# Kernel optimization log

Hardware: AMD Instinct MI355X
Metric: run time of the kernel (lower is better)

## Reference

```python
import jax, jax.numpy as jnp
import numpy as np

# ---- configuration (matches init_kwargs) ----
B, C_IO, T = 2, 64, 4096
PATCH = 2
W0, W1 = 512, 1024           # widths
D_DN, D_MID = 2, 4           # depths per level
DH = 64                      # dim per head
WIN = 128                    # local attention window
MAP = 1024                   # mapping_dim
DFF_MAP = 1024               # mapping_d_ff
FF_MULT = 2                  # GEGLU ff_mult in local levels
H_DN = W0 // DH              # 8 heads
H_MID = W1 // DH             # 16 heads


def _n(key, shape, s=0.02):
    return jax.random.normal(key, shape, jnp.float32) * s


def setup_inputs() -> dict:
    key = jax.random.key(0)
    ks = iter(jax.random.split(key, 64))
    p = {}
    p['x'] = jax.random.normal(next(ks), (B, C_IO, T), jnp.float32)
    p['t'] = jax.random.uniform(next(ks), (B,), jnp.float32)
    p['time_w'] = jax.random.normal(next(ks), (MAP // 2, 1), jnp.float32)
    p['time_in_w'] = _n(next(ks), (MAP, MAP))
    p['map_in_s'] = jnp.ones((MAP,), jnp.float32)
    p['map_norm_s'] = jnp.ones((2, MAP), jnp.float32)
    p['map_up_w'] = _n(next(ks), (2, MAP, 2 * DFF_MAP))
    p['map_down_w'] = _n(next(ks), (2, DFF_MAP, MAP))
    p['map_out_s'] = jnp.ones((MAP,), jnp.float32)
    p['patch_in_w'] = _n(next(ks), (C_IO * PATCH, W0))
    p['dn_anorm_w'] = _n(next(ks), (D_DN, MAP, W0))
    p['dn_qkv_w'] = _n(next(ks), (D_DN, W0, 3 * W0))
    p['dn_o_w'] = _n(next(ks), (D_DN, W0, W0))
    p['dn_fnorm_w'] = _n(next(ks), (D_DN, MAP, W0))
    p['dn_ff1_w'] = _n(next(ks), (D_DN, W0, 2 * FF_MULT * W0))
    p['dn_ff2_w'] = _n(next(ks), (D_DN, FF_MULT * W0, W0))
    p['merge_w'] = _n(next(ks), (W0 * 2, W1))
    p['mid_map_w'] = _n(next(ks), (MAP, W1))
    p['mid_pin_w'] = _n(next(ks), (W1, W1))
    p['mid_pout_w'] = _n(next(ks), (W1, W1))
    p['mid_ln1_g'] = jnp.ones((D_MID, W1), jnp.float32)
    p['mid_ln1_b'] = jnp.zeros((D_MID, W1), jnp.float32)
    p['mid_qkv_w'] = _n(next(ks), (D_MID, W1, 3 * W1))
    p['mid_o_w'] = _n(next(ks), (D_MID, W1, W1))
    p['mid_ln2_g'] = jnp.ones((D_MID, W1), jnp.float32)
    p['mid_ln2_b'] = jnp.zeros((D_MID, W1), jnp.float32)
    p['mid_ff1_w'] = _n(next(ks), (D_MID, W1, 8 * W1))
    p['mid_ff2_w'] = _n(next(ks), (D_MID, 4 * W1, W1))
    p['mid_fn_g'] = jnp.ones((W1,), jnp.float32)
    p['mid_fn_b'] = jnp.zeros((W1,), jnp.float32)
    p['split_w'] = _n(next(ks), (W1, W0 * 2))
    p['split_fac'] = jnp.full((1,), 0.5, jnp.float32)
    p['up_anorm_w'] = _n(next(ks), (D_DN, MAP, W0))
    p['up_qkv_w'] = _n(next(ks), (D_DN, W0, 3 * W0))
    p['up_o_w'] = _n(next(ks), (D_DN, W0, W0))
    p['up_fnorm_w'] = _n(next(ks), (D_DN, MAP, W0))
    p['up_ff1_w'] = _n(next(ks), (D_DN, W0, 2 * FF_MULT * W0))
    p['up_ff2_w'] = _n(next(ks), (D_DN, FF_MULT * W0, W0))
    p['out_norm_s'] = jnp.ones((W0,), jnp.float32)
    p['patch_out_w'] = _n(next(ks), (W0, C_IO * PATCH))
    return p


def rmsnorm(x, scale, eps=1e-6):
    ms = jnp.mean(jnp.square(x), -1, keepdims=True)
    return x * (scale * jax.lax.rsqrt(ms + eps))


def layernorm(x, g, b, eps=1e-5):
    m = jnp.mean(x, -1, keepdims=True)
    v = jnp.mean(jnp.square(x - m), -1, keepdims=True)
    return (x - m) * jax.lax.rsqrt(v + eps) * g + b


def rope_tables(S, D):
    inv = 1.0 / (10000.0 ** (jnp.arange(0, D, 2, dtype=jnp.float32) / D))
    ang = jnp.arange(S, dtype=jnp.float32)[:, None] * inv  # [S, D/2]
    return jnp.cos(ang), jnp.sin(ang)


def apply_rope(x, cos, sin):
    # x: [B,H,S,D], contiguous-half rotation
    x1, x2 = jnp.split(x, 2, -1)
    return jnp.concatenate([x1 * cos - x2 * sin, x2 * cos + x1 * sin], -1)


def heads_split(x, h):
    Bx, S, C = x.shape
    return x.reshape(Bx, S, h, C // h).transpose(0, 2, 1, 3)


def heads_merge(x):
    Bx, h, S, D = x.shape
    return x.transpose(0, 2, 1, 3).reshape(Bx, S, h * D)


def local_attn(q, k, v, w):
    # non-causal sliding-window attention: each query window attends to
    # [prev, self, next] windows (look_backward=1, look_forward=1)
    Bx, H, S, D = q.shape
    nw = S // w
    qw = q.reshape(Bx, H, nw, w, D)
    def ctx(tn):
        tw = tn.reshape(Bx, H, nw, w, D)
        pad = jnp.pad(tw, ((0, 0), (0, 0), (1, 1), (0, 0), (0, 0)))
        return jnp.concatenate([pad[:, :, :-2], pad[:, :, 1:-1], pad[:, :, 2:]], 3)  # [B,H,nw,3w,D]
    kw, vw = ctx(k), ctx(v)
    s = jnp.einsum('bhnqd,bhnkd->bhnqk', qw * (D ** -0.5), kw)
    valid = jnp.ones((nw, 3 * w), bool).at[0, :w].set(False).at[-1, 2 * w:].set(False)
    s = jnp.where(valid[None, None, :, None, :], s, jnp.finfo(s.dtype).min)
    a = jax.nn.softmax(s, -1)
    return jnp.einsum('bhnqk,bhnkd->bhnqd', a, vw).reshape(Bx, H, S, D)


def token_merge(x, w, r=2):
    # 'b (n r) c -> b n (c r)' then linear
    Bx, S, C = x.shape
    x = x.reshape(Bx, S // r, r, C).transpose(0, 1, 3, 2).reshape(Bx, S // r, C * r)
    return x @ w


def token_split(x, w, r=2):
    # linear then 'b n (c r) -> b (n r) c'
    y = x @ w
    Bx, n, CR = y.shape
    C = CR // r
    return y.reshape(Bx, n, C, r).transpose(0, 1, 3, 2).reshape(Bx, n * r, C)


def mapping(e, in_s, norm_s, up_w, down_w, out_s):
    x = rmsnorm(e, in_s)
    for l in range(up_w.shape[0]):
        h = rmsnorm(x, norm_s[l])
        a, g = jnp.split(h @ up_w[l], 2, -1)
        x = x + (a * jax.nn.gelu(g)) @ down_w[l]
    return rmsnorm(x, out_s)


def local_level(x, cond, anorm, qkv_w, o_w, fnorm, ff1, ff2, heads, win):
    Bx, S, C = x.shape
    D = C // heads
    cos, sin = rope_tables(S, D)
    for l in range(qkv_w.shape[0]):
        h = rmsnorm(x, 1.0 + (cond @ anorm[l])[:, None, :])  # AdaRMSNorm
        q, k, v = jnp.split(h @ qkv_w[l], 3, -1)
        q, k, v = heads_split(q, heads), heads_split(k, heads), heads_split(v, heads)
        q, k = apply_rope(q, cos, sin), apply_rope(k, cos, sin)
        x = x + heads_merge(local_attn(q, k, v, win)) @ o_w[l]
        h = rmsnorm(x, 1.0 + (cond @ fnorm[l])[:, None, :])
        a, g = jnp.split(h @ ff1[l], 2, -1)
        x = x + (a * jax.nn.gelu(g)) @ ff2[l]  # GEGLU FF
    return x


def mid_level(x, ln1g, ln1b, qkv_w, o_w, ln2g, ln2b, ff1, ff2, fng, fnb, heads):
    Bx, S, C = x.shape
    D = C // heads
    cos, sin = rope_tables(S, D)
    for l in range(qkv_w.shape[0]):
        h = layernorm(x, ln1g[l], ln1b[l])
        q, k, v = jnp.split(h @ qkv_w[l], 3, -1)
        q, k, v = heads_split(q, heads), heads_split(k, heads), heads_split(v, heads)
        q, k = apply_rope(q, cos, sin), apply_rope(k, cos, sin)
        s = jnp.einsum('bhqd,bhkd->bhqk', q * (D ** -0.5), k)
        o = jnp.einsum('bhqk,bhkd->bhqd', jax.nn.softmax(s, -1), v)
        x = x + heads_merge(o) @ o_w[l]
        h = layernorm(x, ln2g[l], ln2b[l])
        a, g = jnp.split(h @ ff1[l], 2, -1)
        x = x + (a * jax.nn.silu(g)) @ ff2[l]  # SwiGLU FF
    return layernorm(x, fng, fnb)


def _forward(x, t, time_w, time_in_w, map_in_s, map_norm_s, map_up_w, map_down_w, map_out_s,
             patch_in_w, dn_anorm_w, dn_qkv_w, dn_o_w, dn_fnorm_w, dn_ff1_w, dn_ff2_w,
             merge_w, mid_map_w, mid_pin_w, mid_pout_w, mid_ln1_g, mid_ln1_b, mid_qkv_w,
             mid_o_w, mid_ln2_g, mid_ln2_b, mid_ff1_w, mid_ff2_w, mid_fn_g, mid_fn_b,
             split_w, split_fac, up_anorm_w, up_qkv_w, up_o_w, up_fnorm_w, up_ff1_w,
             up_ff2_w, out_norm_s, patch_out_w):
    h = jnp.swapaxes(x, 1, 2)                      # [B,T,C_io]
    h = token_merge(h, patch_in_w, PATCH)          # [B, T/2, W0]
    f = 2.0 * jnp.pi * (t[:, None] @ time_w.T)     # Fourier features
    temb = jnp.concatenate([jnp.cos(f), jnp.sin(f)], -1) @ time_in_w
    cond = mapping(temb, map_in_s, map_norm_s, map_up_w, map_down_w, map_out_s)  # [B,MAP]
    h = local_level(h, cond, dn_anorm_w, dn_qkv_w, dn_o_w, dn_fnorm_w, dn_ff1_w, dn_ff2_w, H_DN, WIN)
    skip = h
    h = token_merge(h, merge_w)                    # [B, T/4, W1]
    h = h @ mid_pin_w
    pre = (cond @ mid_map_w)[:, None, :]           # prepended mapping token
    h = jnp.concatenate([pre, h], 1)
    h = mid_level(h, mid_ln1_g, mid_ln1_b, mid_qkv_w, mid_o_w, mid_ln2_g, mid_ln2_b,
                  mid_ff1_w, mid_ff2_w, mid_fn_g, mid_fn_b, H_MID)
    h = (h @ mid_pout_w)[:, 1:, :]
    h = token_split(h, split_w)                    # back to [B, T/2, W0]
    h = skip + split_fac * (h - skip)              # lerp skip fusion
    h = local_level(h, cond, up_anorm_w, up_qkv_w, up_o_w, up_fnorm_w, up_ff1_w, up_ff2_w, H_DN, WIN)
    h = rmsnorm(h, out_norm_s)
    h = token_split(h, patch_out_w, PATCH)         # [B,T,C_io]
    return jnp.swapaxes(h, 1, 2)


def reference(x, t, time_w, time_in_w, map_in_s, map_norm_s, map_up_w, map_down_w, map_out_s,
              patch_in_w, dn_anorm_w, dn_qkv_w, dn_o_w, dn_fnorm_w, dn_ff1_w, dn_ff2_w,
              merge_w, mid_map_w, mid_pin_w, mid_pout_w, mid_ln1_g, mid_ln1_b, mid_qkv_w,
              mid_o_w, mid_ln2_g, mid_ln2_b, mid_ff1_w, mid_ff2_w, mid_fn_g, mid_fn_b,
              split_w, split_fac, up_anorm_w, up_qkv_w, up_o_w, up_fnorm_w, up_ff1_w,
              up_ff2_w, out_norm_s, patch_out_w):
    return _forward(x, t, time_w, time_in_w, map_in_s, map_norm_s, map_up_w, map_down_w, map_out_s,
                    patch_in_w, dn_anorm_w, dn_qkv_w, dn_o_w, dn_fnorm_w, dn_ff1_w, dn_ff2_w,
                    merge_w, mid_map_w, mid_pin_w, mid_pout_w, mid_ln1_g, mid_ln1_b, mid_qkv_w,
                    mid_o_w, mid_ln2_g, mid_ln2_b, mid_ff1_w, mid_ff2_w, mid_fn_g, mid_fn_b,
                    split_w, split_fac, up_anorm_w, up_qkv_w, up_o_w, up_fnorm_w, up_ff1_w,
                    up_ff2_w, out_norm_s, patch_out_w)
```

## Files before the change

### kernel.cpp

```cpp
#include <hip/hip_runtime.h>
#include <math.h>

#define BB   2
#define CIO  64
#define TT   4096
#define S0   2048
#define W0   512
#define HDN  8
#define SM   1025
#define SMP  1088
#define W1   1024
#define HMID 16
#define WIN  128
#define NW   16
#define MAPD 1024
#define KSPL 16
#define PKCAP 8396800L

typedef _Float16 f16;
typedef _Float16 half8 __attribute__((ext_vector_type(8)));
typedef _Float16 half4v __attribute__((ext_vector_type(4)));
typedef _Float16 half2v __attribute__((ext_vector_type(2)));
typedef float floatx4 __attribute__((ext_vector_type(4)));

__device__ __forceinline__ float gelu_tanh(float x) {
    float x3 = x * x * x;
    return 0.5f * x * (1.f + tanhf(0.7978845608028654f * (x + 0.044715f * x3)));
}

__global__ __launch_bounds__(256) void wcast(
    const float* __restrict__ W, f16* __restrict__ Wt, int K, int N) {
    __shared__ float T[64][65];
    const int n0 = blockIdx.x * 64, k0 = blockIdx.y * 64;
    const int tid = threadIdx.x;
    for (int e = tid; e < 4096; e += 256) {
        int r = e >> 6, c = e & 63;
        T[r][c] = W[(size_t)(k0 + r) * N + n0 + c];
    }
    __syncthreads();
    for (int e = tid; e < 2048; e += 256) {
        int r = e >> 5, c2 = (e & 31) * 2;
        half2v p;
        p[0] = (f16)T[c2][r];
        p[1] = (f16)T[c2 + 1][r];
        *(half2v*)(Wt + (size_t)(n0 + r) * K + k0 + c2) = p;
    }
}

template<int OUTM>
__global__ __launch_bounds__(256) void gemm_h(
    const f16* __restrict__ A, const f16* __restrict__ Bt,
    const float* __restrict__ res, void* __restrict__ Cv,
    int M, int N, int K) {
    __shared__ __align__(16) f16 As[2][4096];
    __shared__ __align__(16) f16 Bs[2][4096];
    const int tid = threadIdx.x;
    const int wv = tid >> 6, ln = tid & 63;
    int nwg = gridDim.x * gridDim.y;
    int orig = blockIdx.y * gridDim.x + blockIdx.x;
    int wg = orig;
    if (nwg >= 16) {
        int q = nwg >> 3, r = nwg & 7;
        int xcd = orig & 7, lot = orig >> 3;
        wg = (xcd < r ? xcd * (q + 1) : r * (q + 1) + (xcd - r) * q) + lot;
    }
    const int bm = (wg / gridDim.x) * 128, bn = (wg % gridDim.x) * 128;
    int Kc = K, kbase = 0;
    if (OUTM == 2) { Kc = K / gridDim.z; kbase = blockIdx.z * Kc; }
    const int nt = Kc >> 5;

    auto stage = [&](int buf, int kt) {
        int k0 = kbase + (kt << 5);
#pragma unroll
        for (int i = 0; i < 2; ++i) {
            int off = i * 4096 + wv * 1024 + ln * 16;
            int row = off >> 6, kb = (off & 63) >> 1;
            int gr = bm + row; gr = gr < M ? gr : M - 1;
            f16* gp = const_cast<f16*>(A) + (size_t)gr * K + k0 + kb;
            __builtin_amdgcn_global_load_lds(
                (__attribute__((address_space(1))) void*)gp,
                (__attribute__((address_space(3))) void*)(&As[buf][i * 2048 + wv * 512]),
                16, 0, 0);
            f16* gq = const_cast<f16*>(Bt) + (size_t)(bn + row) * K + k0 + kb;
            __builtin_amdgcn_global_load_lds(
                (__attribute__((address_space(1))) void*)gq,
                (__attribute__((address_space(3))) void*)(&Bs[buf][i * 2048 + wv * 512]),
                16, 0, 0);
        }
    };

    floatx4 acc[4][4];
#pragma unroll
    for (int m = 0; m < 4; ++m)
#pragma unroll
        for (int n = 0; n < 4; ++n) acc[m][n] = (floatx4)0.f;
    const int r = ln & 15, kc = (ln >> 4) * 8;
    const int wr = (wv >> 1) * 64, wc = (wv & 1) * 64;

    stage(0, 0);
    for (int t = 0; t < nt; ++t) {
        __syncthreads();
        if (t + 1 < nt) stage((t + 1) & 1, t + 1);
        const int buf = t & 1;
        half8 af[4], bf[4];
#pragma unroll
        for (int m = 0; m < 4; ++m)
            af[m] = *(const half8*)(&As[buf][(wr + m * 16 + r) * 32 + kc]);
#pragma unroll
        for (int n = 0; n < 4; ++n)
            bf[n] = *(const half8*)(&Bs[buf][(wc + n * 16 + r) * 32 + kc]);
#pragma unroll
        for (int m = 0; m < 4; ++m)
#pragma unroll
            for (int n = 0; n < 4; ++n)
                acc[m][n] = __builtin_amdgcn_mfma_f32_16x16x32_f16(af[m], bf[n], acc[m][n], 0, 0, 0);
    }

    float* Cf = (float*)Cv;
    f16*   Ch = (f16*)Cv;
    if (OUTM == 2) Cf += (size_t)blockIdx.z * M * N;
#pragma unroll
    for (int m = 0; m < 4; ++m) {
        int rbase = bm + wr + m * 16 + ((ln >> 4) << 2);
#pragma unroll
        for (int j = 0; j < 4; ++j) {
            int row = rbase + j;
            if (row < M) {
                size_t ro = (size_t)row * N;
#pragma unroll
                for (int n = 0; n < 4; ++n) {
                    int col = bn + wc + n * 16 + (ln & 15);
                    float v = acc[m][n][j];
                    if (OUTM == 1) Ch[ro + col] = (f16)v;
                    else if (OUTM == 0) Cf[ro + col] = v + (res ? res[ro + col] : 0.f);
                    else Cf[ro + col] = v;
                }
            }
        }
    }
}

template<bool HOUT>
__global__ __launch_bounds__(256) void kred(
    const float* __restrict__ P, const float* __restrict__ res,
    void* __restrict__ Cv, size_t mn, int ks) {
    size_t i = ((size_t)blockIdx.x * 256 + threadIdx.x) * 4;
    if (i >= mn) return;
    floatx4 s = res ? *(const floatx4*)(res + i) : (floatx4)0.f;
    for (int z = 0; z < ks; ++z) {
        floatx4 p = *(const floatx4*)(P + (size_t)z * mn + i);
        s += p;
    }
    if (HOUT) {
        half4v h;
#pragma unroll
        for (int j = 0; j < 4; ++j) h[j] = (f16)s[j];
        *(half4v*)((f16*)Cv + i) = h;
    } else {
        *(floatx4*)((float*)Cv + i) = s;
    }
}

__global__ __launch_bounds__(256) void gemv2_part(
    const float* __restrict__ A, const float* __restrict__ W,
    float* __restrict__ P, int N, int K) {
    int n = blockIdx.x * 256 + threadIdx.x;
    if (n >= N) return;
    int Kc = K / KSPL;
    int k0 = blockIdx.y * Kc;
    float acc0 = 0.f, acc1 = 0.f;
    const float* Wp = W + (size_t)k0 * N + n;
    const float* a0 = A + k0;
    const float* a1 = A + K + k0;
#pragma unroll 4
    for (int k = 0; k < Kc; ++k) {
        float w = Wp[(size_t)k * N];
        acc0 = fmaf(a0[k], w, acc0);
        acc1 = fmaf(a1[k], w, acc1);
    }
    P[((size_t)blockIdx.y * 2 + 0) * N + n] = acc0;
    P[((size_t)blockIdx.y * 2 + 1) * N + n] = acc1;
}

__global__ __launch_bounds__(256) void gemv2_red(
    const float* __restrict__ P, const float* __restrict__ res,
    float* __restrict__ C, int N) {
    int g = blockIdx.x * 256 + threadIdx.x;
    if (g >= 2 * N) return;
    int m = g / N, n = g - m * N;
    float s = res ? res[g] : 0.f;
#pragma unroll
    for (int ky = 0; ky < KSPL; ++ky)
        s += P[((size_t)ky * 2 + m) * N + n];
    C[g] = s;
}

__device__ __forceinline__ void stf(float* p, float v) { *p = v; }
__device__ __forceinline__ void stf(f16* p, float v)   { *p = (f16)v; }

template<typename TO>
__global__ __launch_bounds__(256) void rmsnorm_k(
    const float* __restrict__ X, const float* __restrict__ scale,
    TO* __restrict__ Y, int C, int rows_per_group, float sadd) {
    int row = blockIdx.x, tid = threadIdx.x;
    const float* x = X + (size_t)row * C;
    float v[8];
    int cnt = C >> 8;
    float ss = 0.f;
    for (int i = 0; i < cnt; ++i) { v[i] = x[tid + (i << 8)]; ss += v[i] * v[i]; }
    __shared__ float red[256];
    red[tid] = ss; __syncthreads();
    for (int s2 = 128; s2; s2 >>= 1) { if (tid < s2) red[tid] += red[tid + s2]; __syncthreads(); }
    float inv = rsqrtf(red[0] / (float)C + 1e-6f);
    const float* sc = scale + (size_t)(row / rows_per_group) * C;
    TO* y = Y + (size_t)row * C;
    for (int i = 0; i < cnt; ++i) {
        int c = tid + (i << 8);
        stf(&y[c], v[i] * (sadd + sc[c]) * inv);
    }
}

__global__ __launch_bounds__(256) void layernorm_k(
    const float* __restrict__ X, const float* __restrict__ g,
    const float* __restrict__ bta, f16* __restrict__ Y, int C) {
    int row = blockIdx.x, tid = threadIdx.x;
    const float* x = X + (size_t)row * C;
    float v[8];
    int cnt = C >> 8;
    float s = 0.f;
    for (int i = 0; i < cnt; ++i) { v[i] = x[tid + (i << 8)]; s += v[i]; }
    __shared__ float red[256];
    red[tid] = s; __syncthreads();
    for (int s2 = 128; s2; s2 >>= 1) { if (tid < s2) red[tid] += red[tid + s2]; __syncthreads(); }
    float m = red[0] / (float)C;
    __syncthreads();
    float s2s = 0.f;
    for (int i = 0; i < cnt; ++i) { float d = v[i] - m; s2s += d * d; }
    red[tid] = s2s; __syncthreads();
    for (int s2 = 128; s2; s2 >>= 1) { if (tid < s2) red[tid] += red[tid + s2]; __syncthreads(); }
    float inv = rsqrtf(red[0] / (float)C + 1e-5f);
    f16* y = Y + (size_t)row * C;
    for (int i = 0; i < cnt; ++i) {
        int c = tid + (i << 8);
        y[c] = (f16)((v[i] - m) * inv * g[c] + bta[c]);
    }
}

__global__ __launch_bounds__(256) void glu_k(
    const float* __restrict__ U, float* __restrict__ Yo,
    size_t total, int F, int mode) {
    size_t gidx = (size_t)blockIdx.x * 256 + threadIdx.x;
    if (gidx >= total) return;
    size_t r = gidx / (size_t)F;
    int c = (int)(gidx - r * F);
    const float* u = U + r * (size_t)(2 * F);
    float a = u[c], gg = u[F + c];
    float act = (mode == 0) ? gelu_tanh(gg) : gg / (1.f + expf(-gg));
    Yo[gidx] = a * act;
}

__global__ __launch_bounds__(256) void glu_h8(
    const f16* __restrict__ U, f16* __restrict__ Yo,
    size_t total8, int F8, int mode) {
    size_t gi = (size_t)blockIdx.x * 256 + threadIdx.x;
    if (gi >= total8) return;
    size_t r = gi / (size_t)F8;
    int c = (int)(gi - r * (size_t)F8);
    const f16* u = U + r * (size_t)F8 * 16;
    half8 av = *(const half8*)(u + c * 8);
    half8 gv = *(const half8*)(u + F8 * 8 + c * 8);
    half8 y;
#pragma unroll
    for (int j = 0; j < 8; ++j) {
        float a = (float)av[j], gg = (float)gv[j];
        float act = (mode == 0) ? gelu_tanh(gg) : gg / (1.f + __expf(-gg));
        y[j] = (f16)(a * act);
    }
    *(half8*)(Yo + gi * 8) = y;
}

__global__ __launch_bounds__(256) void qkv_split_rope(
    const float* __restrict__ QKV, f16* __restrict__ Qo,
    f16* __restrict__ Ko, f16* __restrict__ Vo, int S, int H) {
    int g = blockIdx.x * 256 + threadIdx.x;
    int total = BB * S * H * 32;
    if (g >= total) return;
    int i = g & 31;
    int tix = g >> 5;
    int h = tix % H; tix /= H;
    int s = tix % S; int b = tix / S;
    int C = H * 64;
    const float* base = QKV + (size_t)(b * S + s) * 3 * C + h * 64;
    float q1 = base[i], q2 = base[32 + i];
    float k1 = base[C + i], k2 = base[C + 32 + i];
    float v1 = base[2 * C + i], v2 = base[2 * C + 32 + i];
    float inv = expf(-(float)i * 0.28782313662425575f);
    float ang = (float)s * inv;
    float sn, cs;
    sincosf(ang, &sn, &cs);
    size_t o = ((size_t)(b * H + h) * S + s) * 64 + i;
    Qo[o]      = (f16)((q1 * cs - q2 * sn) * 0.125f);
    Qo[o + 32] = (f16)((q2 * cs + q1 * sn) * 0.125f);
    Ko[o]      = (f16)(k1 * cs - k2 * sn);
    Ko[o + 32] = (f16)(k2 * cs + k1 * sn);
    Vo[o]      = (f16)v1;
    Vo[o + 32] = (f16)v2;
}

__global__ __launch_bounds__(256) void vtrans(
    const f16* __restrict__ V, f16* __restrict__ Vt, int S, int Spad) {
    __shared__ f16 T[64][72];
    const int tid = threadIdx.x;
    const int k0 = blockIdx.x * 64;
    const f16* Vb = V + (size_t)blockIdx.y * S * 64;
    f16* Vtb = Vt + (size_t)blockIdx.y * 64 * Spad;
    for (int c = tid; c < 512; c += 256) {
        int kk = c >> 3, d8 = (c & 7) * 8;
        int kg = k0 + kk; kg = kg < S ? kg : S - 1;
        half8 v = *(const half8*)(Vb + (size_t)kg * 64 + d8);
        if (k0 + kk >= S) {
#pragma unroll
            for (int j = 0; j < 8; ++j) v[j] = (f16)0.f;
        }
        *(half8*)(&T[kk][d8]) = v;
    }
    __syncthreads();
    for (int c = tid; c < 512; c += 256) {
        int d = c >> 3, k8 = (c & 7) * 8;
        half8 o;
#pragma unroll
        for (int j = 0; j < 8; ++j) o[j] = T[k8 + j][d];
        *(half8*)(Vtb + (size_t)d * Spad + k0 + k8) = o;
    }
}

__global__ __launch_bounds__(256) void fattn(
    const f16* __restrict__ Q, const f16* __restrict__ K,
    const f16* __restrict__ Vt, float* __restrict__ Op,
    float* __restrict__ Mst, float* __restrict__ Lst,
    int S, int Spad, int H, int win, int QR) {
    __shared__ __align__(16) f16 Ks[64][72];
    __shared__ __align__(16) f16 Vs[64][72];
    __shared__ __align__(16) f16 Ps[4][32][72];
    const int tid = threadIdx.x;
    const int wv = tid >> 6, ln = tid & 63;
    const int r15 = ln & 15, g = ln >> 4;
    const int bh = blockIdx.y;
    const int NBH = gridDim.y;
    const int z = blockIdx.z, nz = gridDim.z;
    const int q0 = (int)blockIdx.x * 128;
    const f16* Qb = Q + (size_t)bh * S * 64;
    const f16* Kb = K + (size_t)bh * S * 64;
    const f16* Vtb = Vt + (size_t)bh * 64 * Spad;

    half8 aq[2][2];
#pragma unroll
    for (int m = 0; m < 2; ++m) {
        int q = q0 + wv * 32 + m * 16 + r15;
        q = q < S ? q : S - 1;
#pragma unroll
        for (int ks = 0; ks < 2; ++ks)
            aq[m][ks] = *(const half8*)(Qb + (size_t)q * 64 + ks * 32 + g * 8);
    }
    floatx4 o[2][4];
#pragma unroll
    for (int m = 0; m < 2; ++m)
#pragma unroll
        for (int n = 0; n < 4; ++n) o[m][n] = (floatx4)0.f;
    float mst[2][4], lst[2][4];
#pragma unroll
    for (int m = 0; m < 2; ++m)
#pragma unroll
        for (int j = 0; j < 4; ++j) { mst[m][j] = -3.0e38f; lst[m][j] = 0.f; }

    int klo = 0, khi = S;
    if (win) {
        int n = (int)blockIdx.x;
        klo = (n - 1) * win; if (klo < 0) klo = 0;
        khi = (n + 2) * win; if (khi > S) khi = S;
    }
    int ntile = (khi - klo + 63) >> 6;
    int chunk = (ntile + nz - 1) / nz;
    int myLo = klo + z * chunk * 64;
    int myHi = klo + (z + 1) * chunk * 64; if (myHi > khi) myHi = khi;

    for (int kb = myLo; kb < myHi; kb += 64) {
        __syncthreads();
#pragma unroll
        for (int i = 0; i < 2; ++i) {
            int c = tid + i * 256;
            int rr = c >> 3, c8 = (c & 7) * 8;
            int kg = kb + rr; kg = kg < S ? kg : S - 1;
            *(half8*)(&Ks[rr][c8]) = *(const half8*)(Kb + (size_t)kg * 64 + c8);
            *(half8*)(&Vs[rr][c8]) = *(const half8*)(Vtb + (size_t)rr * Spad + kb + c8);
        }
        __syncthreads();
        floatx4 s[2][4];
#pragma unroll
        for (int m = 0; m < 2; ++m)
#pragma unroll
            for (int n = 0; n < 4; ++n) s[m][n] = (floatx4)0.f;
#pragma unroll
        for (int ks = 0; ks < 2; ++ks) {
            half8 bk[4];
#pragma unroll
            for (int n = 0; n < 4; ++n)
                bk[n] = *(const half8*)(&Ks[n * 16 + r15][ks * 32 + g * 8]);
#pragma unroll
            for (int m = 0; m < 2; ++m)
#pragma unroll
                for (int n = 0; n < 4; ++n)
                    s[m][n] = __builtin_amdgcn_mfma_f32_16x16x32_f16(aq[m][ks], bk[n], s[m][n], 0, 0, 0);
        }
        if (kb + 64 > S) {
#pragma unroll
            for (int n = 0; n < 4; ++n)
                if (kb + n * 16 + r15 >= S) {
#pragma unroll
                    for (int m = 0; m < 2; ++m) s[m][n] = (floatx4)(-3.0e38f);
                }
        }
#pragma unroll
        for (int m = 0; m < 2; ++m) {
#pragma unroll
            for (int j = 0; j < 4; ++j) {
                float tm = fmaxf(fmaxf(s[m][0][j], s[m][1][j]), fmaxf(s[m][2][j], s[m][3][j]));
                tm = fmaxf(tm, __shfl_xor(tm, 1));
                tm = fmaxf(tm, __shfl_xor(tm, 2));
                tm = fmaxf(tm, __shfl_xor(tm, 4));
                tm = fmaxf(tm, __shfl_xor(tm, 8));
                float mn = fmaxf(mst[m][j], tm);
                float sc = __expf(mst[m][j] - mn);
                mst[m][j] = mn;
                float ts = 0.f;
#pragma unroll
                for (int n = 0; n < 4; ++n) {
                    float p = __expf(s[m][n][j] - mn);
                    s[m][n][j] = p;
                    ts += p;
                }
                ts += __shfl_xor(ts, 1);
                ts += __shfl_xor(ts, 2);
                ts += __shfl_xor(ts, 4);
                ts += __shfl_xor(ts, 8);
                lst[m][j] = lst[m][j] * sc + ts;
#pragma unroll
                for (int n = 0; n < 4; ++n) o[m][n][j] *= sc;
            }
        }
#pragma unroll
        for (int m = 0; m < 2; ++m)
#pragma unroll
            for (int n = 0; n < 4; ++n)
#pragma unroll
                for (int j = 0; j < 4; ++j)
                    Ps[wv][m * 16 + g * 4 + j][n * 16 + r15] = (f16)s[m][n][j];
#pragma unroll
        for (int ks = 0; ks < 2; ++ks) {
            half8 pa[2], bv[4];
#pragma unroll
            for (int m = 0; m < 2; ++m)
                pa[m] = *(const half8*)(&Ps[wv][m * 16 + r15][ks * 32 + g * 8]);
#pragma unroll
            for (int n = 0; n < 4; ++n)
                bv[n] = *(const half8*)(&Vs[n * 16 + r15][ks * 32 + g * 8]);
#pragma unroll
            for (int m = 0; m < 2; ++m)
#pragma unroll
                for (int n = 0; n < 4; ++n)
                    o[m][n] = __builtin_amdgcn_mfma_f32_16x16x32_f16(pa[m], bv[n], o[m][n], 0, 0, 0);
        }
    }
    size_t zb = ((size_t)z * NBH + bh) * QR;
#pragma unroll
    for (int m = 0; m < 2; ++m)
#pragma unroll
        for (int j = 0; j < 4; ++j) {
            int qr = q0 + wv * 32 + m * 16 + g * 4 + j;
            size_t ro = (zb + qr) * 64;
#pragma unroll
            for (int n = 0; n < 4; ++n)
                Op[ro + n * 16 + r15] = o[m][n][j];
            if (r15 == 0) {
                Mst[zb + qr] = mst[m][j];
                Lst[zb + qr] = lst[m][j];
            }
        }
}

__global__ __launch_bounds__(256) void fcomb(
    const float* __restrict__ Op, const float* __restrict__ Mst,
    const float* __restrict__ Lst, f16* __restrict__ O,
    int S, int H, int QR, int nz, int rows) {
    int g = blockIdx.x * 256 + threadIdx.x;
    int idx = g >> 4;
    int d4 = (g & 15) * 4;
    if (idx >= rows) return;
    int bh = idx / QR, q = idx - bh * QR;
    if (q >= S) return;
    float mstar = -3.0e38f;
    for (int z = 0; z < nz; ++z)
        mstar = fmaxf(mstar, Mst[(size_t)z * rows + idx]);
    float den = 0.f;
    floatx4 num = (floatx4)0.f;
    for (int z = 0; z < nz; ++z) {
        float w = __expf(Mst[(size_t)z * rows + idx] - mstar);
        den += w * Lst[(size_t)z * rows + idx];
        floatx4 ov = *(const floatx4*)(Op + ((size_t)z * rows + idx) * 64 + d4);
        num += w * ov;
    }
    float inv = 1.f / den;
    int b = bh / H, h = bh % H;
    f16* op = O + ((size_t)b * S + q) * (H * 64) + h * 64 + d4;
    half4v hv;
#pragma unroll
    for (int j = 0; j < 4; ++j) hv[j] = (f16)(num[j] * inv);
    *(half4v*)op = hv;
}

__global__ __launch_bounds__(256) void patch_in_gather(
    const float* __restrict__ x, f16* __restrict__ out) {
    int g = blockIdx.x * 256 + threadIdx.x;
    if (g >= BB * S0 * 128) return;
    int k = g & 127;
    int n = (g >> 7) & (S0 - 1);
    int b = g >> 18;
    out[g] = (f16)x[(size_t)b * CIO * TT + (size_t)(k >> 1) * TT + 2 * n + (k & 1)];
}

__global__ __launch_bounds__(256) void time_embed(
    const float* __restrict__ t, const float* __restrict__ tw,
    float* __restrict__ te) {
    int g = blockIdx.x * 256 + threadIdx.x;
    if (g >= BB * MAPD) return;
    int b = g / MAPD, j = g % MAPD;
    float w = tw[(j < 512) ? j : j - 512];
    float ang = 6.283185307179586f * t[b] * w;
    te[g] = (j < 512) ? cosf(ang) : sinf(ang);
}

__global__ __launch_bounds__(256) void token_merge_gather(
    const float* __restrict__ A, f16* __restrict__ out) {
    int g = blockIdx.x * 256 + threadIdx.x;
    if (g >= BB * 1024 * 1024) return;
    int k = g & 1023;
    int n = (g >> 10) & 1023;
    int b = g >> 20;
    out[g] = (f16)A[((size_t)b * S0 + 2 * n + (k & 1)) * W0 + (k >> 1)];
}

__global__ __launch_bounds__(256) void concat_mid(
    const float* __restrict__ pre, const float* __restrict__ Dsrc,
    float* __restrict__ Cm) {
    int g = blockIdx.x * 256 + threadIdx.x;
    if (g >= BB * SM * W1) return;
    int c = g & 1023;
    int row = g >> 10;
    int b = row / SM, r = row % SM;
    Cm[g] = (r == 0) ? pre[b * W1 + c]
                     : Dsrc[((size_t)b * 1024 + r - 1) * W1 + c];
}

__global__ __launch_bounds__(256) void gather_drop(
    const f16* __restrict__ Dsrc, f16* __restrict__ out) {
    int g = blockIdx.x * 256 + threadIdx.x;
    if (g >= BB * 1024 * W1) return;
    int c = g & 1023;
    int n = (g >> 10) & 1023;
    int b = g >> 20;
    out[g] = Dsrc[((size_t)b * SM + 1 + n) * W1 + c];
}

__global__ __launch_bounds__(256) void split_scatter_lerp(
    const float* __restrict__ y, const float* __restrict__ skip,
    const float* __restrict__ fac, float* __restrict__ xo) {
    int g = blockIdx.x * 256 + threadIdx.x;
    if (g >= BB * S0 * W0) return;
    int c = g & 511;
    int tk = (g >> 9) & (S0 - 1);
    int b = g >> 20;
    float yv = y[((size_t)b * 1024 + (tk >> 1)) * W1 + (c * 2 + (tk & 1))];
    float sk = skip[g];
    xo[g] = sk + fac[0] * (yv - sk);
}

__global__ __launch_bounds__(256) void patch_out_scatter(
    const float* __restrict__ y, float* __restrict__ out) {
    int g = blockIdx.x * 256 + threadIdx.x;
    if (g >= BB * CIO * TT) return;
    int tk = g & (TT - 1);
    int c = (g >> 12) & 63;
    int b = g >> 18;
    out[g] = y[((size_t)b * S0 + (tk >> 1)) * 128 + (c * 2 + (tk & 1))];
}

extern "C" void kernel_launch(void* const* d_in, const int* in_sizes, int n_in,
                              void* d_out, int out_size, void* d_ws, size_t ws_size,
                              hipStream_t stream) {
    const float* x          = (const float*)d_in[0];
    const float* t          = (const float*)d_in[1];
    const float* time_w     = (const float*)d_in[2];
    const float* time_in_w  = (const float*)d_in[3];
    const float* map_in_s   = (const float*)d_in[4];
    const float* map_norm_s = (const float*)d_in[5];
    const float* map_up_w   = (const float*)d_in[6];
    const float* map_down_w = (const float*)d_in[7];
    const float* map_out_s  = (const float*)d_in[8];
    const float* patch_in_w = (const float*)d_in[9];
    const float* dn_anorm_w = (const float*)d_in[10];
    const float* dn_qkv_w   = (const float*)d_in[11];
    const float* dn_o_w     = (const float*)d_in[12];
    const float* dn_fnorm_w = (const float*)d_in[13];
    const float* dn_ff1_w   = (const float*)d_in[14];
    const float* dn_ff2_w   = (const float*)d_in[15];
    const float* merge_w    = (const float*)d_in[16];
    const float* mid_map_w  = (const float*)d_in[17];
    const float* mid_pin_w  = (const float*)d_in[18];
    const float* mid_pout_w = (const float*)d_in[19];
    const float* mid_ln1_g  = (const float*)d_in[20];
    const float* mid_ln1_b  = (const float*)d_in[21];
    const float* mid_qkv_w  = (const float*)d_in[22];
    const float* mid_o_w    = (const float*)d_in[23];
    const float* mid_ln2_g  = (const float*)d_in[24];
    const float* mid_ln2_b  = (const float*)d_in[25];
    const float* mid_ff1_w  = (const float*)d_in[26];
    const float* mid_ff2_w  = (const float*)d_in[27];
    const float* mid_fn_g   = (const float*)d_in[28];
    const float* mid_fn_b   = (const float*)d_in[29];
    const float* split_w    = (const float*)d_in[30];
    const float* split_fac  = (const float*)d_in[31];
    const float* up_anorm_w = (const float*)d_in[32];
    const float* up_qkv_w   = (const float*)d_in[33];
    const float* up_o_w     = (const float*)d_in[34];
    const float* up_fnorm_w = (const float*)d_in[35];
    const float* up_ff1_w   = (const float*)d_in[36];
    const float* up_ff2_w   = (const float*)d_in[37];
    const float* out_norm_s = (const float*)d_in[38];
    const float* patch_out_w= (const float*)d_in[39];

    float* Wp = (float*)d_ws;
    size_t off = 0;
    auto alloc = [&](size_t n) { float* p = Wp + off; off += n; return p; };
    float* A   = alloc((size_t)4096 * 512);
    float* Bsk = alloc((size_t)4096 * 512);
    float* Cm  = alloc((size_t)2050 * 1024);
    float* Df  = alloc((size_t)2050 * 1024);
    float* E32 = alloc((size_t)2050 * 3072);
    f16*  Fq   = (f16*)alloc((size_t)1049600);
    f16*  Fk   = (f16*)alloc((size_t)1049600);
    f16*  Fv   = (f16*)alloc((size_t)1049600);
    f16*  Fvt  = (f16*)alloc((size_t)1114112);
    f16*  H1   = (f16*)alloc((size_t)8396800);
    f16*  H2   = (f16*)alloc((size_t)4198400);
    f16*  Wh   = (f16*)alloc((size_t)4194304);
    float* Pk  = alloc((size_t)PKCAP);
    float* ML  = alloc((size_t)262144);
    float* Pb  = alloc((size_t)KSPL * 2 * 2048);
    float* Sma = alloc((size_t)32768);
    (void)ws_size; (void)in_sizes; (void)n_in; (void)out_size;

    float* te   = Sma;
    float* temb = Sma + 2048;
    float* mapx = Sma + 4096;
    float* maph = Sma + 6144;
    float* mapu = Sma + 8192;
    float* mapg = Sma + 12288;
    float* cond = Sma + 14336;
    float* sA   = Sma + 16384;
    float* sF   = Sma + 17408;
    float* pre  = Sma + 18432;

    auto WC = [&](const float* W, int K, int N) {
        wcast<<<dim3(N / 64, K / 64), 256, 0, stream>>>(W, Wh, K, N);
    };
    auto pick_ks = [](int M, int N, int K) {
        long gx = N / 128, gy = (M + 127) / 128;
        int ks = 1;
        while (gx * gy * ks < 512 && ks < 8) {
            int nk = ks * 2;
            if ((K / nk) % 32 != 0 || (long)M * N * nk > PKCAP) break;
            ks = nk;
        }
        return ks;
    };
    auto GF = [&](const f16* Aa, const float* res, float* C, int M, int N, int K) {
        int ks = pick_ks(M, N, K);
        dim3 g(N / 128, (M + 127) / 128, ks);
        if (ks == 1) {
            gemm_h<0><<<g, 256, 0, stream>>>(Aa, Wh, res, C, M, N, K);
        } else {
            gemm_h<2><<<g, 256, 0, stream>>>(Aa, Wh, nullptr, Pk, M, N, K);
            size_t mn = (size_t)M * N;
            kred<false><<<(int)((mn / 4 + 255) / 256), 256, 0, stream>>>(Pk, res, C, mn, ks);
        }
    };
    auto GH = [&](const f16* Aa, f16* C, int M, int N, int K) {
        int ks = pick_ks(M, N, K);
        dim3 g(N / 128, (M + 127) / 128, ks);
        if (ks == 1) {
            gemm_h<1><<<g, 256, 0, stream>>>(Aa, Wh, nullptr, C, M, N, K);
        } else {
            gemm_h<2><<<g, 256, 0, stream>>>(Aa, Wh, nullptr, Pk, M, N, K);
            size_t mn = (size_t)M * N;
            kred<true><<<(int)((mn / 4 + 255) / 256), 256, 0, stream>>>(Pk, nullptr, C, mn, ks);
        }
    };
    auto gemv2 = [&](const float* Aa, const float* W, const float* res,
                     float* C, int N, int K) {
        gemv2_part<<<dim3((N + 255) / 256, KSPL), 256, 0, stream>>>(Aa, W, Pb, N, K);
        gemv2_red<<<(2 * N + 255) / 256, 256, 0, stream>>>(Pb, res, C, N);
    };
    auto FATT = [&](const f16* Qp, const f16* Kp, const f16* Vtp, f16* Out,
                    int S, int Spad, int H, int win, int nq, int nbh, int nz) {
        int QR = nq * 128;
        int rows = nbh * QR;
        fattn<<<dim3(nq, nbh, nz), 256, 0, stream>>>(
            Qp, Kp, Vtp, Pk, ML, ML + (size_t)nz * rows, S, Spad, H, win, QR);
        fcomb<<<(rows * 16 + 255) / 256, 256, 0, stream>>>(
            Pk, ML, ML + (size_t)nz * rows, Out, S, H, QR, nz, rows);
    };

    patch_in_gather<<<(BB * S0 * 128 + 255) / 256, 256, 0, stream>>>(x, H2);
    WC(patch_in_w, 128, 512);
    GF(H2, nullptr, A, 4096, 512, 128);

    time_embed<<<(BB * MAPD + 255) / 256, 256, 0, stream>>>(t, time_w, te);
    gemv2(te, time_in_w, nullptr, temb, 1024, 1024);
    rmsnorm_k<float><<<2, 256, 0, stream>>>(temb, map_in_s, mapx, 1024, 2, 0.f);
    for (int l = 0; l < 2; ++l) {
        rmsnorm_k<float><<<2, 256, 0, stream>>>(mapx, map_norm_s + (size_t)l * 1024, maph, 1024, 2, 0.f);
        gemv2(maph, map_up_w + (size_t)l * 1024 * 2048, nullptr, mapu, 2048, 1024);
        glu_k<<<(2 * 1024 + 255) / 256, 256, 0, stream>>>(mapu, mapg, 2 * 1024, 1024, 0);
        gemv2(mapg, map_down_w + (size_t)l * 1024 * 1024, mapx, mapx, 1024, 1024);
    }
    rmsnorm_k<float><<<2, 256, 0, stream>>>(mapx, map_out_s, cond, 1024, 2, 0.f);

    auto run_local = [&](const float* anorm, const float* qkvw, const float* ow,
                         const float* fnorm, const float* ff1, const float* ff2) {
        for (int l = 0; l < 2; ++l) {
            gemv2(cond, anorm + (size_t)l * 1024 * 512, nullptr, sA, 512, 1024);
            rmsnorm_k<f16><<<4096, 256, 0, stream>>>(A, sA, H2, 512, 2048, 1.f);
            WC(qkvw + (size_t)l * 512 * 1536, 512, 1536);
            GF(H2, nullptr, E32, 4096, 1536, 512);
            qkv_split_rope<<<(BB * S0 * HDN * 32 + 255) / 256, 256, 0, stream>>>(E32, Fq, Fk, Fv, S0, HDN);
            vtrans<<<dim3(S0 / 64, BB * HDN), 256, 0, stream>>>(Fv, Fvt, S0, S0);
            FATT(Fq, Fk, Fvt, H2, S0, S0, HDN, WIN, S0 / 128, BB * HDN, 2);
            WC(ow + (size_t)l * 512 * 512, 512, 512);
            GF(H2, A, A, 4096, 512, 512);
            gemv2(cond, fnorm + (size_t)l * 1024 * 512, nullptr, sF, 512, 1024);
            rmsnorm_k<f16><<<4096, 256, 0, stream>>>(A, sF, H2, 512, 2048, 1.f);
            WC(ff1 + (size_t)l * 512 * 2048, 512, 2048);
            GH(H2, H1, 4096, 2048, 512);
            glu_h8<<<(4096 * 128 + 255) / 256, 256, 0, stream>>>(H1, H2, (size_t)4096 * 128, 128, 0);
            WC(ff2 + (size_t)l * 1024 * 512, 1024, 512);
            GF(H2, A, A, 4096, 512, 1024);
        }
    };
    run_local(dn_anorm_w, dn_qkv_w, dn_o_w, dn_fnorm_w, dn_ff1_w, dn_ff2_w);

    hipMemcpyAsync(Bsk, A, (size_t)4096 * 512 * 4, hipMemcpyDeviceToDevice, stream);
    token_merge_gather<<<(BB * 1024 * 1024 + 255) / 256, 256, 0, stream>>>(A, H2);
    WC(merge_w, 1024, 1024);
    GH(H2, H1, 2048, 1024, 1024);
    WC(mid_pin_w, 1024, 1024);
    GF(H1, nullptr, Df, 2048, 1024, 1024);
    gemv2(cond, mid_map_w, nullptr, pre, 1024, 1024);
    concat_mid<<<(BB * SM * W1 + 255) / 256, 256, 0, stream>>>(pre, Df, Cm);

    for (int l = 0; l < 4; ++l) {
        layernorm_k<<<2050, 256, 0, stream>>>(Cm, mid_ln1_g + (size_t)l * 1024,
                                              mid_ln1_b + (size_t)l * 1024, H2, 1024);
        WC(mid_qkv_w + (size_t)l * 1024 * 3072, 1024, 3072);
        GF(H2, nullptr, E32, 2050, 3072, 1024);
        qkv_split_rope<<<(BB * SM * HMID * 32 + 255) / 256, 256, 0, stream>>>(E32, Fq, Fk, Fv, SM, HMID);
        vtrans<<<dim3(SMP / 64, BB * HMID), 256, 0, stream>>>(Fv, Fvt, SM, SMP);
        FATT(Fq, Fk, Fvt, H2, SM, SMP, HMID, 0, 9, BB * HMID, 3);
        WC(mid_o_w + (size_t)l * 1024 * 1024, 1024, 1024);
        GF(H2, Cm, Cm, 2050, 1024, 1024);
        layernorm_k<<<2050, 256, 0, stream>>>(Cm, mid_ln2_g + (size_t)l * 1024,
                                              mid_ln2_b + (size_t)l * 1024, H2, 1024);
        WC(mid_ff1_w + (size_t)l * 1024 * 8192, 1024, 8192);
        GH(H2, H1, 2050, 8192, 1024);
        glu_h8<<<(int)(((size_t)2050 * 512 + 255) / 256), 256, 0, stream>>>(H1, H2, (size_t)2050 * 512, 512, 1);
        WC(mid_ff2_w + (size_t)l * 4096 * 1024, 4096, 1024);
        GF(H2, Cm, Cm, 2050, 1024, 4096);
    }
    layernorm_k<<<2050, 256, 0, stream>>>(Cm, mid_fn_g, mid_fn_b, H2, 1024);

    WC(mid_pout_w, 1024, 1024);
    GH(H2, H1, 2050, 1024, 1024);
    gather_drop<<<(BB * 1024 * W1 + 255) / 256, 256, 0, stream>>>(H1, H2);
    WC(split_w, 1024, 1024);
    GF(H2, nullptr, Df, 2048, 1024, 1024);
    split_scatter_lerp<<<(BB * S0 * W0 + 255) / 256, 256, 0, stream>>>(Df, Bsk, split_fac, A);

    run_local(up_anorm_w, up_qkv_w, up_o_w, up_fnorm_w, up_ff1_w, up_ff2_w);

    rmsnorm_k<f16><<<4096, 256, 0, stream>>>(A, out_norm_s, H2, 512, 4096, 0.f);
    WC(patch_out_w, 512, 128);
    GF(H2, nullptr, Df, 4096, 128, 512);
    patch_out_scatter<<<(BB * CIO * TT + 255) / 256, 256, 0, stream>>>(Df, (float*)d_out);
}
```

Before: 2.146 ms.

## Triple-buffer GEMM LDS pipeline and emit QKV projections in fp16

The GEMM main loop goes from double to triple buffering in LDS. It prefetches two K-tiles ahead and uses explicit vmcnt waits with a bare barrier instead of __syncthreads, so global-to-LDS loads overlap more with MFMA work. Separately, the QKV projection GEMMs now write fp16 into an existing half buffer instead of fp32, which roughly halves the write and read traffic into the rope/split kernel and removes the fp32 scratch buffer. Costs are higher LDS use per block (possible occupancy loss) and an extra fp16 rounding of Q/K before rope.

```diff
diff --git a/kernel.cpp b/kernel.cpp
--- a/kernel.cpp
+++ b/kernel.cpp
@@ -52,8 +52,8 @@
     const f16* __restrict__ A, const f16* __restrict__ Bt,
     const float* __restrict__ res, void* __restrict__ Cv,
     int M, int N, int K) {
-    __shared__ __align__(16) f16 As[2][4096];
-    __shared__ __align__(16) f16 Bs[2][4096];
+    __shared__ __align__(16) f16 As[3][4096];
+    __shared__ __align__(16) f16 Bs[3][4096];
     const int tid = threadIdx.x;
     const int wv = tid >> 6, ln = tid & 63;
     int nwg = gridDim.x * gridDim.y;
@@ -98,10 +98,16 @@
     const int wr = (wv >> 1) * 64, wc = (wv & 1) * 64;
 
     stage(0, 0);
+    if (nt > 1) stage(1, 1);
+    int buf = 0;
     for (int t = 0; t < nt; ++t) {
-        __syncthreads();
-        if (t + 1 < nt) stage((t + 1) & 1, t + 1);
-        const int buf = t & 1;
+        if (t + 1 < nt) { asm volatile("s_waitcnt vmcnt(4)" ::: "memory"); }
+        else            { asm volatile("s_waitcnt vmcnt(0)" ::: "memory"); }
+        __builtin_amdgcn_s_barrier();
+        if (t + 2 < nt) {
+            int nb = buf + 2; if (nb >= 3) nb -= 3;
+            stage(nb, t + 2);
+        }
         half8 af[4], bf[4];
 #pragma unroll
         for (int m = 0; m < 4; ++m)
@@ -114,6 +120,7 @@
 #pragma unroll
             for (int n = 0; n < 4; ++n)
                 acc[m][n] = __builtin_amdgcn_mfma_f32_16x16x32_f16(af[m], bf[n], acc[m][n], 0, 0, 0);
+        if (++buf >= 3) buf = 0;
     }
 
     float* Cf = (float*)Cv;
@@ -280,7 +287,7 @@
 }
 
 __global__ __launch_bounds__(256) void qkv_split_rope(
-    const float* __restrict__ QKV, f16* __restrict__ Qo,
+    const f16* __restrict__ QKV, f16* __restrict__ Qo,
     f16* __restrict__ Ko, f16* __restrict__ Vo, int S, int H) {
     int g = blockIdx.x * 256 + threadIdx.x;
     int total = BB * S * H * 32;
@@ -290,10 +297,10 @@
     int h = tix % H; tix /= H;
     int s = tix % S; int b = tix / S;
     int C = H * 64;
-    const float* base = QKV + (size_t)(b * S + s) * 3 * C + h * 64;
-    float q1 = base[i], q2 = base[32 + i];
-    float k1 = base[C + i], k2 = base[C + 32 + i];
-    float v1 = base[2 * C + i], v2 = base[2 * C + 32 + i];
+    const f16* base = QKV + (size_t)(b * S + s) * 3 * C + h * 64;
+    float q1 = (float)base[i], q2 = (float)base[32 + i];
+    float k1 = (float)base[C + i], k2 = (float)base[C + 32 + i];
+    f16 v1 = base[2 * C + i], v2 = base[2 * C + 32 + i];
     float inv = expf(-(float)i * 0.28782313662425575f);
     float ang = (float)s * inv;
     float sn, cs;
@@ -303,8 +310,8 @@
     Qo[o + 32] = (f16)((q2 * cs + q1 * sn) * 0.125f);
     Ko[o]      = (f16)(k1 * cs - k2 * sn);
     Ko[o + 32] = (f16)(k2 * cs + k1 * sn);
-    Vo[o]      = (f16)v1;
-    Vo[o + 32] = (f16)v2;
+    Vo[o]      = v1;
+    Vo[o + 32] = v2;
 }
 
 __global__ __launch_bounds__(256) void vtrans(
@@ -645,7 +652,6 @@
     float* Bsk = alloc((size_t)4096 * 512);
     float* Cm  = alloc((size_t)2050 * 1024);
     float* Df  = alloc((size_t)2050 * 1024);
-    float* E32 = alloc((size_t)2050 * 3072);
     f16*  Fq   = (f16*)alloc((size_t)1049600);
     f16*  Fk   = (f16*)alloc((size_t)1049600);
     f16*  Fv   = (f16*)alloc((size_t)1049600);
@@ -741,8 +747,8 @@
             gemv2(cond, anorm + (size_t)l * 1024 * 512, nullptr, sA, 512, 1024);
             rmsnorm_k<f16><<<4096, 256, 0, stream>>>(A, sA, H2, 512, 2048, 1.f);
             WC(qkvw + (size_t)l * 512 * 1536, 512, 1536);
-            GF(H2, nullptr, E32, 4096, 1536, 512);
-            qkv_split_rope<<<(BB * S0 * HDN * 32 + 255) / 256, 256, 0, stream>>>(E32, Fq, Fk, Fv, S0, HDN);
+            GH(H2, H1, 4096, 1536, 512);
+            qkv_split_rope<<<(BB * S0 * HDN * 32 + 255) / 256, 256, 0, stream>>>(H1, Fq, Fk, Fv, S0, HDN);
             vtrans<<<dim3(S0 / 64, BB * HDN), 256, 0, stream>>>(Fv, Fvt, S0, S0);
             FATT(Fq, Fk, Fvt, H2, S0, S0, HDN, WIN, S0 / 128, BB * HDN, 2);
             WC(ow + (size_t)l * 512 * 512, 512, 512);
@@ -771,8 +777,8 @@
         layernorm_k<<<2050, 256, 0, stream>>>(Cm, mid_ln1_g + (size_t)l * 1024,
                                               mid_ln1_b + (size_t)l * 1024, H2, 1024);
         WC(mid_qkv_w + (size_t)l * 1024 * 3072, 1024, 3072);
-        GF(H2, nullptr, E32, 2050, 3072, 1024);
-        qkv_split_rope<<<(BB * SM * HMID * 32 + 255) / 256, 256, 0, stream>>>(E32, Fq, Fk, Fv, SM, HMID);
+        GH(H2, H1, 2050, 3072, 1024);
+        qkv_split_rope<<<(BB * SM * HMID * 32 + 255) / 256, 256, 0, stream>>>(H1, Fq, Fk, Fv, SM, HMID);
         vtrans<<<dim3(SMP / 64, BB * HMID), 256, 0, stream>>>(Fv, Fvt, SM, SMP);
         FATT(Fq, Fk, Fvt, H2, SM, SMP, HMID, 0, 9, BB * HMID, 3);
         WC(mid_o_w + (size_t)l * 1024 * 1024, 1024, 1024);
```

New measurement: 2.110 ms. About the same (-1.7%).
